# Kernel tuning notes

Hardware: AMD Instinct MI355X
Metric: run time of the kernel (lower is better)

Reference implementation:

```python
import jax, jax.numpy as jnp
import numpy as np
from jax import lax

T = 4          # timesteps (leading batch dim is T * effective_batch)
NUM_HEAD = 8
TAU = 0.5      # LIF membrane leak
THRESH = 1.0   # firing threshold
GAMA = 1.0     # surrogate-gradient width (ZIF)
SCALE = 0.125
EPS = 1e-5     # BatchNorm eps

@jax.custom_vjp
def zif(x):
    # Heaviside spike with triangular surrogate gradient (ZIF from TET/SNN repos)
    return (x > 0.0).astype(x.dtype)

def _zif_fwd(x):
    return zif(x), x

def _zif_bwd(x, g):
    tmp = (1.0 / GAMA) ** 2 * jnp.clip(GAMA - jnp.abs(x), 0.0)
    return (g * tmp,)

zif.defvjp(_zif_fwd, _zif_bwd)

def lif(x):
    # x: [T*B, C, N]; leaky-integrate-fire scan over T timesteps
    TB = x.shape[0]
    xt = x.reshape(T, TB // T, *x.shape[1:])
    def step(mem, xi):
        mem = mem * TAU + xi
        s = zif(mem - THRESH)
        return (1.0 - s) * mem, s  # hard reset
    _, spikes = lax.scan(step, jnp.zeros_like(xt[0]), xt)
    return spikes.reshape(x.shape)

def conv_bn(x, w, gamma, beta, mean, var):
    # 1x1 Conv1d (channel matmul) fused with eval-mode BatchNorm1d
    y = jnp.einsum('oc,bcn->bon', w, x)
    inv = gamma / jnp.sqrt(var + EPS)
    return y * inv[None, :, None] + (beta - mean * inv)[None, :, None]

def setup_inputs():
    key = jax.random.key(0)
    ks = jax.random.split(key, 9)
    C, B, N = 512, 64, 512
    s = 1.0 / np.sqrt(C)
    return {
        "x": jax.random.normal(ks[0], (B, C, N), jnp.float32),
        "wq": jax.random.normal(ks[1], (C, C), jnp.float32) * s,
        "wk": jax.random.normal(ks[2], (C, C), jnp.float32) * s,
        "wv": jax.random.normal(ks[3], (C, C), jnp.float32) * s,
        "wproj": jax.random.normal(ks[4], (C, C), jnp.float32) * s,
        "bn_gamma": 1.0 + 0.1 * jax.random.normal(ks[5], (4, C), jnp.float32),
        "bn_beta": 0.1 * jax.random.normal(ks[6], (4, C), jnp.float32),
        "bn_mean": 0.1 * jax.random.normal(ks[7], (4, C), jnp.float32),
        "bn_var": 0.5 + jax.random.uniform(ks[8], (4, C), jnp.float32),
    }

def reference(x, wq, wk, wv, wproj, bn_gamma, bn_beta, bn_mean, bn_var):
    B, C, N = x.shape
    gd = C // NUM_HEAD
    q = lif(conv_bn(x, wq, bn_gamma[0], bn_beta[0], bn_mean[0], bn_var[0]))
    k = lif(conv_bn(x, wk, bn_gamma[1], bn_beta[1], bn_mean[1], bn_var[1]))
    v = lif(conv_bn(x, wv, bn_gamma[2], bn_beta[2], bn_mean[2], bn_var[2]))
    q = q.reshape(B, NUM_HEAD, gd, N)
    k = k.reshape(B, NUM_HEAD, gd, N)
    v = v.reshape(B, NUM_HEAD, gd, N)
    # q.permute(0,1,3,2) @ k -> [B,H,N,N]  (softmax-free spiking attention)
    attn = jnp.einsum('bhdn,bhdm->bhnm', q, k) * SCALE
    # attn @ v.permute(0,1,3,2), then permute back -> [B,H,gd,N]
    out = jnp.einsum('bhnm,bhdm->bhdn', attn, v)
    out = out.reshape(B, C, N)
    out = lif(out)
    return conv_bn(out, wproj, bn_gamma[3], bn_beta[3], bn_mean[3], bn_var[3])
```

## Files before the change

kernel.cpp:

```cpp
#include <hip/hip_runtime.h>
#include <hip/hip_bf16.h>
#include <stdint.h>

#define TT 4
#define BE 16
#define BB 64
#define CC 512
#define NN 512
#define NH 8
#define GD 64
#define NW 16
#define TAU 0.5f
#define THRESH 1.0f
#define SCALE 0.125f
#define EPS 1e-5f

typedef _Float16 half8 __attribute__((ext_vector_type(8)));
typedef float    f32x4 __attribute__((ext_vector_type(4)));

#define GLL16(g, l)                                                        \
    __builtin_amdgcn_global_load_lds(                                      \
        (const __attribute__((address_space(1))) void*)(g),                \
        (__attribute__((address_space(3))) void*)(l), 16, 0, 0)

__global__ __launch_bounds__(256) void split_w_kernel(
    const float* __restrict__ wq, const float* __restrict__ wk,
    const float* __restrict__ wv, const float* __restrict__ wp,
    _Float16* __restrict__ Wpk)
{
    const int gid = blockIdx.x * 256 + threadIdx.x;
    const int k8  = gid & 63;
    const int c   = (gid >> 6) & 511;
    const int mat = gid >> 15;
    const float* src = (mat == 0) ? wq : (mat == 1) ? wk : (mat == 2) ? wv : wp;
    const float* p = src + (size_t)c * CC + k8 * 8;
    float4 a = *(const float4*)p;
    float4 bq = *(const float4*)(p + 4);
    half8 h, l;
    h[0] = (_Float16)a.x;  l[0] = (_Float16)(a.x  - (float)h[0]);
    h[1] = (_Float16)a.y;  l[1] = (_Float16)(a.y  - (float)h[1]);
    h[2] = (_Float16)a.z;  l[2] = (_Float16)(a.z  - (float)h[2]);
    h[3] = (_Float16)a.w;  l[3] = (_Float16)(a.w  - (float)h[3]);
    h[4] = (_Float16)bq.x; l[4] = (_Float16)(bq.x - (float)h[4]);
    h[5] = (_Float16)bq.y; l[5] = (_Float16)(bq.y - (float)h[5]);
    h[6] = (_Float16)bq.z; l[6] = (_Float16)(bq.z - (float)h[6]);
    h[7] = (_Float16)bq.w; l[7] = (_Float16)(bq.w - (float)h[7]);
    const size_t uh = ((((size_t)(mat * 4 + (c >> 7)) * 16 + (k8 >> 2)) * 16
                      + ((c >> 4) & 7)) * 64) + (size_t)((k8 & 3) * 16 + (c & 15));
    *(half8*)&Wpk[uh * 8] = h;
    *(half8*)&Wpk[(uh + 8 * 64) * 8] = l;
}

__global__ __launch_bounds__(256) void split_xt_kernel(
    const float* __restrict__ x, _Float16* __restrict__ Xpk)
{
    __shared__ float Ls[64][68];
    const int tid = threadIdx.x;
    const int b  = blockIdx.z;
    const int k0 = blockIdx.y * 64;
    const int nt = blockIdx.x;
    const float* xb = x + ((size_t)b * CC + k0) * NN + nt * 64;

    const int kr = tid >> 4;
    const int f4 = tid & 15;
#pragma unroll
    for (int i = 0; i < 4; ++i) {
        float4 v = *(const float4*)&xb[(size_t)(kr + 16 * i) * NN + f4 * 4];
        *(float4*)&Ls[kr + 16 * i][f4 * 4] = v;
    }
    __syncthreads();

    const int nr = tid >> 2;
    const int ks = tid & 3;
    const size_t base = ((size_t)b * 8 + nt) * 16;
    const int sX = nr >> 4;
    const int lnlo = nr & 15;

#pragma unroll
    for (int half = 0; half < 2; ++half) {
        half8 h, l;
#pragma unroll
        for (int j = 0; j < 8; ++j) {
            float v = Ls[ks * 16 + half * 8 + j][nr];
            _Float16 hh = (_Float16)v;
            h[j] = hh; l[j] = (_Float16)(v - (float)hh);
        }
        const int k = k0 + ks * 16 + half * 8;
        const int kt = k >> 5, g = (k >> 3) & 3;
        const size_t uh = ((base + kt) * 8 + sX) * 64 + g * 16 + lnlo;
        const size_t ul = ((base + kt) * 8 + 4 + sX) * 64 + g * 16 + lnlo;
        *(half8*)&Xpk[uh * 8] = h;
        *(half8*)&Xpk[ul * 8] = l;
    }
}

__global__ __launch_bounds__(256) void conv_mfma_kernel(
    const _Float16* __restrict__ Wpk,
    const _Float16* __restrict__ Xpk,
    const float* __restrict__ bn_g,
    const float* __restrict__ bn_b,
    const float* __restrict__ bn_m,
    const float* __restrict__ bn_v,
    uint32_t* __restrict__ qp,
    uint32_t* __restrict__ kp,
    uint32_t* __restrict__ vp)
{
    __shared__ _Float16 T[24 * 512];

    const int tid = threadIdx.x;
    const int lane = tid & 63;
    const int wid  = tid >> 6;
    const int wr = wid >> 1;
    const int wc = wid & 1;
    const int lr = lane & 15;
    const int g  = lane >> 4;
    const int lane8 = lane * 8;

    const int hw = blockIdx.x + (blockIdx.y << 3) + (blockIdx.z << 5);
    const int lg = (hw & 7) * 192 + (hw >> 3);
    const int nt = lg & 7;
    const int n0 = nt * 64;
    const int ct = (lg >> 3) & 3;
    const int c0 = ct * 128;
    const int z  = lg >> 5;
    const int be = z & (BE - 1);
    const int wmat = z >> 4;

    uint32_t* outp = (wmat == 0) ? qp : (wmat == 1) ? kp : vp;

    const size_t wst0 = (size_t)(wmat * 4 + ct) * 16;

    f32x4 mem[4][2];
#pragma unroll
    for (int mf = 0; mf < 4; ++mf)
#pragma unroll
        for (int nf = 0; nf < 2; ++nf) mem[mf][nf] = (f32x4)0.0f;

#pragma unroll 1
    for (int t = 0; t < TT; ++t) {
        const int b = t * BE + be;
        const size_t xst0 = ((size_t)b * 8 + nt) * 16;

        f32x4 acc[4][2];
#pragma unroll
        for (int mf = 0; mf < 4; ++mf)
#pragma unroll
            for (int nf = 0; nf < 2; ++nf) acc[mf][nf] = (f32x4)0.0f;

#pragma unroll 1
        for (int kt = 0; kt < 16; ++kt) {
            __syncthreads();
            const size_t wb = (wst0 + kt) * 1024;
            const size_t xb = (xst0 + kt) * 512;
            GLL16(Wpk + (wb + (size_t)(wid)      * 64 + lane) * 8, &T[(wid +  0) * 512]);
            GLL16(Wpk + (wb + (size_t)(wid +  4) * 64 + lane) * 8, &T[(wid +  4) * 512]);
            GLL16(Wpk + (wb + (size_t)(wid +  8) * 64 + lane) * 8, &T[(wid +  8) * 512]);
            GLL16(Wpk + (wb + (size_t)(wid + 12) * 64 + lane) * 8, &T[(wid + 12) * 512]);
            GLL16(Xpk + (xb + (size_t)(wid)      * 64 + lane) * 8, &T[(16 + wid) * 512]);
            GLL16(Xpk + (xb + (size_t)(4 + wid)  * 64 + lane) * 8, &T[(20 + wid) * 512]);
            __syncthreads();

            half8 ah[4], al[4], bh[2], bl[2];
#pragma unroll
            for (int mf = 0; mf < 4; ++mf) {
                ah[mf] = *(const half8*)&T[(wr * 4 + mf) * 512 + lane8];
                al[mf] = *(const half8*)&T[(8 + wr * 4 + mf) * 512 + lane8];
            }
#pragma unroll
            for (int nf = 0; nf < 2; ++nf) {
                bh[nf] = *(const half8*)&T[(16 + wc * 2 + nf) * 512 + lane8];
                bl[nf] = *(const half8*)&T[(20 + wc * 2 + nf) * 512 + lane8];
            }
#pragma unroll
            for (int mf = 0; mf < 4; ++mf)
#pragma unroll
                for (int nf = 0; nf < 2; ++nf) {
                    acc[mf][nf] = __builtin_amdgcn_mfma_f32_16x16x32_f16(
                        ah[mf], bh[nf], acc[mf][nf], 0, 0, 0);
                    acc[mf][nf] = __builtin_amdgcn_mfma_f32_16x16x32_f16(
                        ah[mf], bl[nf], acc[mf][nf], 0, 0, 0);
                    acc[mf][nf] = __builtin_amdgcn_mfma_f32_16x16x32_f16(
                        al[mf], bh[nf], acc[mf][nf], 0, 0, 0);
                }
        }

        const int nword = (n0 >> 5) + wc;
#pragma unroll
        for (int mf = 0; mf < 4; ++mf) {
#pragma unroll
            for (int r = 0; r < 4; ++r) {
                const int c = c0 + wr * 64 + mf * 16 + 4 * g + r;
                const float gg = bn_g[wmat * CC + c];
                const float bb = bn_b[wmat * CC + c];
                const float mm = bn_m[wmat * CC + c];
                const float vv = bn_v[wmat * CC + c];
                const float inv = gg / sqrtf(vv + EPS);
                const float add = bb - mm * inv;

                float y0 = acc[mf][0][r] * inv + add;
                float m0 = mem[mf][0][r] * TAU + y0;
                bool s0 = m0 > THRESH;
                mem[mf][0][r] = s0 ? 0.0f : m0;

                float y1 = acc[mf][1][r] * inv + add;
                float m1 = mem[mf][1][r] * TAU + y1;
                bool s1 = m1 > THRESH;
                mem[mf][1][r] = s1 ? 0.0f : m1;

                uint32_t wbits = ((s0 ? 1u : 0u) << lr) |
                                 ((s1 ? 1u : 0u) << (16 + lr));
                wbits |= (uint32_t)__shfl_xor((int)wbits, 1);
                wbits |= (uint32_t)__shfl_xor((int)wbits, 2);
                wbits |= (uint32_t)__shfl_xor((int)wbits, 4);
                wbits |= (uint32_t)__shfl_xor((int)wbits, 8);
                if (lr == 0) {
                    outp[(size_t)(b * CC + c) * NW + nword] = wbits;
                }
            }
        }
    }
}

__global__ __launch_bounds__(256) void attn_lif_kernel(
    const uint32_t* __restrict__ qp,
    const uint32_t* __restrict__ kp,
    const uint32_t* __restrict__ vp,
    uint32_t* __restrict__ s3p)
{
    __shared__ uint32_t kL[64][NW + 1];
    __shared__ uint32_t vL[64][NW + 1];
    __shared__ float    Msh[64][64 + 1];
    __shared__ uint32_t qL[64][5];

    const int tid = threadIdx.x;
    const int nchunk = blockIdx.x;
    const int h = blockIdx.y;
    const int be = blockIdx.z;
    const int d_own = tid >> 2;
    const int nw_own = tid & 3;

    float mem[32];
#pragma unroll
    for (int i = 0; i < 32; ++i) mem[i] = 0.0f;

    for (int t = 0; t < TT; ++t) {
        const int b = t * BE + be;
        const size_t base_row = (size_t)(b * CC + h * GD);

        for (int i = tid; i < 64 * NW; i += 256) {
            int r = i >> 4;
            int w = i & (NW - 1);
            kL[r][w] = kp[(base_row + r) * NW + w];
            vL[r][w] = vp[(base_row + r) * NW + w];
        }
        {
            int r = tid >> 2;
            int w = tid & 3;
            qL[r][w] = qp[(base_row + r) * NW + nchunk * 4 + w];
        }
        __syncthreads();

        for (int e = tid; e < 64 * 64; e += 256) {
            int d = e >> 6;
            int dp = e & 63;
            int s = 0;
#pragma unroll
            for (int w = 0; w < NW; ++w) s += __popc(vL[d][w] & kL[dp][w]);
            Msh[d][dp] = (float)s;
        }
        __syncthreads();

        float acc[32];
#pragma unroll
        for (int i = 0; i < 32; ++i) acc[i] = 0.0f;

        for (int dp = 0; dp < 64; ++dp) {
            float Mv = Msh[d_own][dp];
            uint32_t w = qL[dp][nw_own];
#pragma unroll
            for (int b2 = 0; b2 < 32; ++b2) {
                acc[b2] += ((w >> b2) & 1u) ? Mv : 0.0f;
            }
        }

        uint32_t sw = 0;
#pragma unroll
        for (int b2 = 0; b2 < 32; ++b2) {
            float m2 = mem[b2] * TAU + SCALE * acc[b2];
            bool s = m2 > THRESH;
            sw |= (s ? 1u : 0u) << b2;
            mem[b2] = s ? 0.0f : m2;
        }
        s3p[(base_row + d_own) * NW + nchunk * 4 + nw_own] = sw;
        __syncthreads();
    }
}

__global__ __launch_bounds__(256) void unpack_kernel(
    const uint32_t* __restrict__ s3p, _Float16* __restrict__ Spk)
{
    __shared__ uint32_t Wd[64][NW + 1];
    const int tid = threadIdx.x;
    const int c0 = blockIdx.x * 64;
    const int b  = blockIdx.y;
    const uint32_t* sp = s3p + ((size_t)b * CC + c0) * NW;

#pragma unroll
    for (int s = 0; s < 4; ++s) {
        int i = tid + s * 256;
        Wd[i >> 4][i & 15] = sp[i];
    }
    __syncthreads();

#pragma unroll
    for (int s = 0; s < 2; ++s) {
        const int n = tid + s * 256;
        const int nw = n >> 5, bit = n & 31;
        const size_t base = ((size_t)b * 8 + (n >> 6)) * 16;
        const int sX = (n >> 4) & 3;
        const int lnlo = n & 15;
#pragma unroll
        for (int c8 = 0; c8 < 8; ++c8) {
            half8 h;
#pragma unroll
            for (int j = 0; j < 8; ++j)
                h[j] = ((Wd[c8 * 8 + j][nw] >> bit) & 1u) ? (_Float16)1.0f
                                                          : (_Float16)0.0f;
            const int k = c0 + c8 * 8;
            const int kt = k >> 5, g = (k >> 3) & 3;
            const size_t u = ((base + kt) * 4 + sX) * 64 + g * 16 + lnlo;
            *(half8*)&Spk[u * 8] = h;
        }
    }
}

__global__ __launch_bounds__(256) void proj_mfma_kernel(
    const _Float16* __restrict__ Wpk,
    const _Float16* __restrict__ Spk,
    const float* __restrict__ bn_g,
    const float* __restrict__ bn_b,
    const float* __restrict__ bn_m,
    const float* __restrict__ bn_v,
    float* __restrict__ out)
{
    __shared__ _Float16 P[12 * 512];

    const int tid = threadIdx.x;
    const int lane = tid & 63;
    const int wid  = tid >> 6;
    const int wr = wid >> 1;
    const int wc = wid & 1;
    const int lr = lane & 15;
    const int g  = lane >> 4;
    const int lane8 = lane * 8;

    const int hw = blockIdx.x + (blockIdx.y << 3) + (blockIdx.z << 5);
    const int lg = (hw & 7) * 256 + (hw >> 3);
    const int nt = lg & 7;
    const int n0 = nt * 64;
    const int ct = (lg >> 3) & 3;
    const int c0 = ct * 128;
    const int b  = lg >> 5;

    const size_t wst0 = (size_t)(3 * 4 + ct) * 16;
    const size_t sst0 = ((size_t)b * 8 + nt) * 16;

    f32x4 acc[4][2];
#pragma unroll
    for (int mf = 0; mf < 4; ++mf)
#pragma unroll
        for (int nf = 0; nf < 2; ++nf) acc[mf][nf] = (f32x4)0.0f;

#pragma unroll 1
    for (int kt = 0; kt < 16; ++kt) {
        __syncthreads();
        const size_t wb = (wst0 + kt) * 1024;
        const size_t sb = (sst0 + kt) * 256;
        GLL16(Wpk + (wb + (size_t)(wid)     * 64 + lane) * 8, &P[(wid + 0) * 512]);
        GLL16(Wpk + (wb + (size_t)(wid + 4) * 64 + lane) * 8, &P[(wid + 4) * 512]);
        GLL16(Spk + (sb + (size_t)(wid)     * 64 + lane) * 8, &P[(8 + wid) * 512]);
        __syncthreads();

        half8 ah[4], bh[2];
#pragma unroll
        for (int mf = 0; mf < 4; ++mf)
            ah[mf] = *(const half8*)&P[(wr * 4 + mf) * 512 + lane8];
#pragma unroll
        for (int nf = 0; nf < 2; ++nf)
            bh[nf] = *(const half8*)&P[(8 + wc * 2 + nf) * 512 + lane8];
#pragma unroll
        for (int mf = 0; mf < 4; ++mf)
#pragma unroll
            for (int nf = 0; nf < 2; ++nf)
                acc[mf][nf] = __builtin_amdgcn_mfma_f32_16x16x32_f16(
                    ah[mf], bh[nf], acc[mf][nf], 0, 0, 0);
    }

    float* ob = out + (size_t)b * CC * NN;
#pragma unroll
    for (int mf = 0; mf < 4; ++mf) {
#pragma unroll
        for (int r = 0; r < 4; ++r) {
            const int c = c0 + wr * 64 + mf * 16 + 4 * g + r;
            const float gg = bn_g[3 * CC + c];
            const float bb = bn_b[3 * CC + c];
            const float mm = bn_m[3 * CC + c];
            const float vv = bn_v[3 * CC + c];
            const float inv = gg / sqrtf(vv + EPS);
            const float add = bb - mm * inv;
            ob[(size_t)c * NN + n0 + wc * 32 + lr]      = acc[mf][0][r] * inv + add;
            ob[(size_t)c * NN + n0 + wc * 32 + 16 + lr] = acc[mf][1][r] * inv + add;
        }
    }
}

extern "C" void kernel_launch(void* const* d_in, const int* in_sizes, int n_in,
                              void* d_out, int out_size, void* d_ws, size_t ws_size,
                              hipStream_t stream) {
    const float* x     = (const float*)d_in[0];
    const float* wq    = (const float*)d_in[1];
    const float* wk    = (const float*)d_in[2];
    const float* wv    = (const float*)d_in[3];
    const float* wproj = (const float*)d_in[4];
    const float* bng   = (const float*)d_in[5];
    const float* bnb   = (const float*)d_in[6];
    const float* bnm   = (const float*)d_in[7];
    const float* bnv   = (const float*)d_in[8];

    uint8_t* ws = (uint8_t*)d_ws;
    const size_t PK = (size_t)BB * CC * NW;
    uint32_t* qp  = (uint32_t*)ws;
    uint32_t* kp  = qp + PK;
    uint32_t* vp  = kp + PK;
    uint32_t* s3p = vp + PK;
    _Float16* Wpk = (_Float16*)(ws + ((size_t)8  << 20));
    _Float16* Xpk = (_Float16*)(ws + ((size_t)12 << 20));
    _Float16* Spk = Xpk;

    split_w_kernel<<<512, 256, 0, stream>>>(wq, wk, wv, wproj, Wpk);
    split_xt_kernel<<<dim3(8, 8, BB), 256, 0, stream>>>(x, Xpk);

    dim3 gconv(NN / 64, CC / 128, 3 * BE);
    conv_mfma_kernel<<<gconv, 256, 0, stream>>>(Wpk, Xpk,
                                                bng, bnb, bnm, bnv, qp, kp, vp);

    dim3 gattn(4, NH, BE);
    attn_lif_kernel<<<gattn, 256, 0, stream>>>(qp, kp, vp, s3p);

    unpack_kernel<<<dim3(CC / 64, BB), 256, 0, stream>>>(s3p, Spk);

    dim3 gproj(NN / 64, CC / 128, BB);
    proj_mfma_kernel<<<gproj, 256, 0, stream>>>(Wpk, Spk,
                                                bng, bnb, bnm, bnv, (float*)d_out);
}
```

Baseline: 668.2 us.

## Reuse weight tile across all four timesteps in conv kernel

```diff
diff --git a/kernel.cpp b/kernel.cpp
--- a/kernel.cpp
+++ b/kernel.cpp
@@ -105,7 +105,7 @@
     uint32_t* __restrict__ kp,
     uint32_t* __restrict__ vp)
 {
-    __shared__ _Float16 T[24 * 512];
+    __shared__ _Float16 T[48 * 512];
 
     const int tid = threadIdx.x;
     const int lane = tid & 63;
@@ -136,73 +136,83 @@
 #pragma unroll
         for (int nf = 0; nf < 2; ++nf) mem[mf][nf] = (f32x4)0.0f;
 
+    f32x4 acc[4][4][2];
+#pragma unroll
+    for (int tl = 0; tl < 4; ++tl)
+#pragma unroll
+        for (int mf = 0; mf < 4; ++mf)
+#pragma unroll
+            for (int nf = 0; nf < 2; ++nf) acc[tl][mf][nf] = (f32x4)0.0f;
+
 #pragma unroll 1
-    for (int t = 0; t < TT; ++t) {
-        const int b = t * BE + be;
-        const size_t xst0 = ((size_t)b * 8 + nt) * 16;
-
-        f32x4 acc[4][2];
-#pragma unroll
-        for (int mf = 0; mf < 4; ++mf)
-#pragma unroll
-            for (int nf = 0; nf < 2; ++nf) acc[mf][nf] = (f32x4)0.0f;
-
-#pragma unroll 1
-        for (int kt = 0; kt < 16; ++kt) {
-            __syncthreads();
-            const size_t wb = (wst0 + kt) * 1024;
-            const size_t xb = (xst0 + kt) * 512;
-            GLL16(Wpk + (wb + (size_t)(wid)      * 64 + lane) * 8, &T[(wid +  0) * 512]);
-            GLL16(Wpk + (wb + (size_t)(wid +  4) * 64 + lane) * 8, &T[(wid +  4) * 512]);
-            GLL16(Wpk + (wb + (size_t)(wid +  8) * 64 + lane) * 8, &T[(wid +  8) * 512]);
-            GLL16(Wpk + (wb + (size_t)(wid + 12) * 64 + lane) * 8, &T[(wid + 12) * 512]);
-            GLL16(Xpk + (xb + (size_t)(wid)      * 64 + lane) * 8, &T[(16 + wid) * 512]);
-            GLL16(Xpk + (xb + (size_t)(4 + wid)  * 64 + lane) * 8, &T[(20 + wid) * 512]);
-            __syncthreads();
-
-            half8 ah[4], al[4], bh[2], bl[2];
-#pragma unroll
-            for (int mf = 0; mf < 4; ++mf) {
-                ah[mf] = *(const half8*)&T[(wr * 4 + mf) * 512 + lane8];
-                al[mf] = *(const half8*)&T[(8 + wr * 4 + mf) * 512 + lane8];
+    for (int kt = 0; kt < 16; ++kt) {
+        __syncthreads();
+        const size_t wb = (wst0 + kt) * 1024;
+        GLL16(Wpk + (wb + (size_t)(wid)      * 64 + lane) * 8, &T[(wid +  0) * 512]);
+        GLL16(Wpk + (wb + (size_t)(wid +  4) * 64 + lane) * 8, &T[(wid +  4) * 512]);
+        GLL16(Wpk + (wb + (size_t)(wid +  8) * 64 + lane) * 8, &T[(wid +  8) * 512]);
+        GLL16(Wpk + (wb + (size_t)(wid + 12) * 64 + lane) * 8, &T[(wid + 12) * 512]);
+#pragma unroll
+        for (int tl = 0; tl < 4; ++tl) {
+            const size_t xb =
+                (((size_t)(tl * BE + be) * 8 + nt) * 16 + kt) * 512;
+            GLL16(Xpk + (xb + (size_t)(wid)     * 64 + lane) * 8,
+                  &T[(16 + tl * 8 + wid) * 512]);
+            GLL16(Xpk + (xb + (size_t)(4 + wid) * 64 + lane) * 8,
+                  &T[(16 + tl * 8 + 4 + wid) * 512]);
+        }
+        __syncthreads();
+
+        half8 ah[4], al[4];
+#pragma unroll
+        for (int mf = 0; mf < 4; ++mf) {
+            ah[mf] = *(const half8*)&T[(wr * 4 + mf) * 512 + lane8];
+            al[mf] = *(const half8*)&T[(8 + wr * 4 + mf) * 512 + lane8];
+        }
+#pragma unroll
+        for (int tl = 0; tl < 4; ++tl) {
+            half8 bh[2], bl[2];
+#pragma unroll
+            for (int nf = 0; nf < 2; ++nf) {
+                bh[nf] = *(const half8*)&T[(16 + tl * 8 + wc * 2 + nf) * 512 + lane8];
+                bl[nf] = *(const half8*)&T[(20 + tl * 8 + wc * 2 + nf) * 512 + lane8];
             }
 #pragma unroll
-            for (int nf = 0; nf < 2; ++nf) {
-                bh[nf] = *(const half8*)&T[(16 + wc * 2 + nf) * 512 + lane8];
-                bl[nf] = *(const half8*)&T[(20 + wc * 2 + nf) * 512 + lane8];
-            }
-#pragma unroll
             for (int mf = 0; mf < 4; ++mf)
 #pragma unroll
                 for (int nf = 0; nf < 2; ++nf) {
-                    acc[mf][nf] = __builtin_amdgcn_mfma_f32_16x16x32_f16(
-                        ah[mf], bh[nf], acc[mf][nf], 0, 0, 0);
-                    acc[mf][nf] = __builtin_amdgcn_mfma_f32_16x16x32_f16(
-                        ah[mf], bl[nf], acc[mf][nf], 0, 0, 0);
-                    acc[mf][nf] = __builtin_amdgcn_mfma_f32_16x16x32_f16(
-                        al[mf], bh[nf], acc[mf][nf], 0, 0, 0);
+                    acc[tl][mf][nf] = __builtin_amdgcn_mfma_f32_16x16x32_f16(
+                        ah[mf], bh[nf], acc[tl][mf][nf], 0, 0, 0);
+                    acc[tl][mf][nf] = __builtin_amdgcn_mfma_f32_16x16x32_f16(
+                        ah[mf], bl[nf], acc[tl][mf][nf], 0, 0, 0);
+                    acc[tl][mf][nf] = __builtin_amdgcn_mfma_f32_16x16x32_f16(
+                        al[mf], bh[nf], acc[tl][mf][nf], 0, 0, 0);
                 }
         }
-
-        const int nword = (n0 >> 5) + wc;
-#pragma unroll
-        for (int mf = 0; mf < 4; ++mf) {
-#pragma unroll
-            for (int r = 0; r < 4; ++r) {
-                const int c = c0 + wr * 64 + mf * 16 + 4 * g + r;
-                const float gg = bn_g[wmat * CC + c];
-                const float bb = bn_b[wmat * CC + c];
-                const float mm = bn_m[wmat * CC + c];
-                const float vv = bn_v[wmat * CC + c];
-                const float inv = gg / sqrtf(vv + EPS);
-                const float add = bb - mm * inv;
-
-                float y0 = acc[mf][0][r] * inv + add;
+    }
+
+    const int nword = (n0 >> 5) + wc;
+#pragma unroll
+    for (int mf = 0; mf < 4; ++mf) {
+#pragma unroll
+        for (int r = 0; r < 4; ++r) {
+            const int c = c0 + wr * 64 + mf * 16 + 4 * g + r;
+            const float gg = bn_g[wmat * CC + c];
+            const float bb = bn_b[wmat * CC + c];
+            const float mm = bn_m[wmat * CC + c];
+            const float vv = bn_v[wmat * CC + c];
+            const float inv = gg / sqrtf(vv + EPS);
+            const float add = bb - mm * inv;
+#pragma unroll
+            for (int tl = 0; tl < 4; ++tl) {
+                const int b = tl * BE + be;
+
+                float y0 = acc[tl][mf][0][r] * inv + add;
                 float m0 = mem[mf][0][r] * TAU + y0;
                 bool s0 = m0 > THRESH;
                 mem[mf][0][r] = s0 ? 0.0f : m0;
 
-                float y1 = acc[mf][1][r] * inv + add;
+                float y1 = acc[tl][mf][1][r] * inv + add;
                 float m1 = mem[mf][1][r] * TAU + y1;
                 bool s1 = m1 > THRESH;
                 mem[mf][1][r] = s1 ? 0.0f : m1;
```

New measurement: 545.9 us. 18.3% less time.
